# Kernel optimization log

Measured on AMD Instinct MI355X. Metric: run time of the kernel, lower is better.

The kernel has to match this reference:

```python
import jax, jax.numpy as jnp
import numpy as np

DIM = 256
N_EMBED = 8192
DECAY = 0.1
COMMITMENT = 1.0
EPS = 1e-05


def setup_inputs() -> dict:
    key = jax.random.key(0)
    k1, k2, k3, k4 = jax.random.split(key, 4)
    return {
        "input": jax.random.normal(k1, (8, 1024, DIM), dtype=jnp.float32),
        "embed": jax.random.normal(k2, (DIM, N_EMBED), dtype=jnp.float32),
        "cluster_size": jax.random.uniform(k3, (N_EMBED,), dtype=jnp.float32),
        "embed_avg": jax.random.normal(k4, (DIM, N_EMBED), dtype=jnp.float32),
    }


def reference(input, embed, cluster_size, embed_avg):
    dtype = input.dtype
    flatten = input.reshape(-1, DIM)  # [N, dim]
    # squared euclidean distance to each code: [N, n_embed]
    dist = (
        jnp.sum(flatten * flatten, axis=1, keepdims=True)
        - 2.0 * (flatten @ embed)
        + jnp.sum(embed * embed, axis=0, keepdims=True)
    )
    embed_ind_flat = jnp.argmin(dist, axis=1)  # [N]
    embed_ind = embed_ind_flat.reshape(input.shape[:-1])
    quantize = jnp.take(embed.T, embed_ind, axis=0)  # [..., dim]

    # EMA codebook update (training path), via segment sums instead of dense one-hot
    bins = jax.ops.segment_sum(
        jnp.ones_like(embed_ind_flat, dtype=dtype), embed_ind_flat, num_segments=N_EMBED
    )  # one_hot.sum(0)
    embed_sum = jax.ops.segment_sum(flatten, embed_ind_flat, num_segments=N_EMBED).T  # [dim, n_embed]
    cluster_size_new = cluster_size * DECAY + (1.0 - DECAY) * bins
    embed_avg_new = embed_avg * DECAY + (1.0 - DECAY) * embed_sum
    smoothed = (cluster_size_new + EPS) / (jnp.sum(cluster_size_new) + N_EMBED * EPS)
    cs = smoothed * jnp.sum(cluster_size_new)
    embed_normalized = embed_avg_new / cs[None, :]

    commit_loss = jnp.mean((jax.lax.stop_gradient(quantize) - input) ** 2) * COMMITMENT
    quantize_st = input + jax.lax.stop_gradient(quantize - input)
    return (quantize_st, embed_ind, commit_loss, embed_normalized, cluster_size_new, embed_avg_new)
```

## Files before the change

### kernel.cpp

```cpp
#include <hip/hip_runtime.h>

typedef unsigned short u16;
typedef __attribute__((ext_vector_type(8))) short short8;
typedef __attribute__((ext_vector_type(4))) float f32x4;

#define DIM    256
#define NE     8192
#define NROWS  8192
#define DECAY  0.1f
#define EPS_F  1e-5f
#define CRANGES 16
#define CPAIRS  16
#define MQ      384u

#define OUT_Q    0
#define OUT_IND  2097152
#define OUT_LOSS 2105344
#define OUT_NORM 2105345
#define OUT_CSN  4202497
#define OUT_AVG  4210689

#define WS_CAND  65536
#define WS_ENORM 1114112
#define WS_BASEQ 1146880
#define WS_SUM   1179648
#define WS_BINS  9568256
#define WS_LOSS  9601024
#define WS_SCS   9601032
#define WS_XB    9601040
#define WS_ETB   13795344
#define WS_ET32  17989648
#define WS_ZLEN  (WS_XB - WS_SUM)

__device__ __forceinline__ unsigned f32_ord(float f)
{
    unsigned u = __float_as_uint(f);
    return (u & 0x80000000u) ? ~u : (u | 0x80000000u);
}
__device__ __forceinline__ u16 bf16rne(float f)
{
    unsigned u = __float_as_uint(f);
    return (u16)((u + 0x7fffu + ((u >> 16) & 1u)) >> 16);
}
__device__ __forceinline__ void gload16(const void* g, void* l)
{
    __builtin_amdgcn_global_load_lds((const __attribute__((address_space(1))) unsigned int*)g,
                                     (__attribute__((address_space(3))) unsigned int*)l, 16, 0, 0);
}

__global__ __launch_bounds__(256) void vq_prep_k(const float* __restrict__ X,
                                                 const float* __restrict__ E,
                                                 const float* __restrict__ CS,
                                                 u16* __restrict__ Xb,
                                                 float* __restrict__ ET32,
                                                 u16* __restrict__ ETb,
                                                 float* __restrict__ enorm,
                                                 float* __restrict__ baseq,
                                                 double* __restrict__ sumcs)
{
    const int bid = blockIdx.x;
    const int t = threadIdx.x;

    if (bid < 128) {
        __shared__ float T[64][65];
        const int j0 = bid * 64;
        const int jc = t >> 2, seg = t & 3;
        const int j = j0 + jc;
        float esum = 0.f;
        for (int d0 = 0; d0 < DIM; d0 += 64) {
            if (d0) __syncthreads();
            #pragma unroll
            for (int p = 0; p < 4; ++p) {
                const int dr = p * 16 + (t >> 4);
                const float4 v = *(const float4*)(E + (size_t)(d0 + dr) * NE + j0 + (t & 15) * 4);
                T[dr][(t & 15) * 4 + 0] = v.x; T[dr][(t & 15) * 4 + 1] = v.y;
                T[dr][(t & 15) * 4 + 2] = v.z; T[dr][(t & 15) * 4 + 3] = v.w;
            }
            __syncthreads();
            float vals[16];
            #pragma unroll
            for (int i = 0; i < 16; ++i) vals[i] = T[seg * 16 + i][jc];
            float4* o32 = (float4*)(ET32 + (size_t)j * DIM + d0 + seg * 16);
            o32[0] = make_float4(vals[0], vals[1], vals[2], vals[3]);
            o32[1] = make_float4(vals[4], vals[5], vals[6], vals[7]);
            o32[2] = make_float4(vals[8], vals[9], vals[10], vals[11]);
            o32[3] = make_float4(vals[12], vals[13], vals[14], vals[15]);
            short8 b0, b1;
            #pragma unroll
            for (int i = 0; i < 8; ++i) { b0[i] = (short)bf16rne(vals[i]); b1[i] = (short)bf16rne(vals[8 + i]); }
            *(short8*)(ETb + (size_t)j * DIM + d0 + seg * 16) = b0;
            *(short8*)(ETb + (size_t)j * DIM + d0 + seg * 16 + 8) = b1;
            #pragma unroll
            for (int i = 0; i < 16; ++i) esum += vals[i] * vals[i];
        }
        esum += __shfl_xor(esum, 1, 4);
        esum += __shfl_xor(esum, 2, 4);
        if (seg == 0) {
            enorm[j] = esum;
            baseq[j] = (esum + 512.f) * 256.f;
        }
    } else if (bid < 256) {
        const int chunk = bid - 128;
        #pragma unroll
        for (int it = 0; it < 8; ++it) {
            const int gi = chunk * 2048 + it * 256 + t;
            const float4 a = ((const float4*)X)[gi * 2];
            const float4 b = ((const float4*)X)[gi * 2 + 1];
            short8 v;
            v[0] = (short)bf16rne(a.x); v[1] = (short)bf16rne(a.y);
            v[2] = (short)bf16rne(a.z); v[3] = (short)bf16rne(a.w);
            v[4] = (short)bf16rne(b.x); v[5] = (short)bf16rne(b.y);
            v[6] = (short)bf16rne(b.z); v[7] = (short)bf16rne(b.w);
            *(short8*)(Xb + (size_t)gi * 8) = v;
        }
    } else {
        double s = 0.0;
        #pragma unroll
        for (int it = 0; it < 8; ++it) {
            const float4 v = ((const float4*)CS)[it * 256 + t];
            s += (double)v.x + (double)v.y + (double)v.z + (double)v.w;
        }
        #pragma unroll
        for (int off = 32; off > 0; off >>= 1) s += __shfl_down(s, off);
        __shared__ double wred[4];
        if ((t & 63) == 0) wred[t >> 6] = s;
        __syncthreads();
        if (t == 0) sumcs[0] = wred[0] + wred[1] + wred[2] + wred[3];
    }
}

__global__ __launch_bounds__(256, 4) void vq_scan_k(const u16* __restrict__ Xb,
                                                    const u16* __restrict__ ETb,
                                                    const float* __restrict__ baseq,
                                                    unsigned* __restrict__ cand)
{
    __shared__ u16 Bs[2][16][512];

    const int tid = threadIdx.x;
    const int w = tid >> 6, l = tid & 63;
    const int lane16 = l & 15, g = l >> 4;
    const int rowbase = blockIdx.x * 128 + w * 32;
    const int c0 = blockIdx.y * 512;

    short8 af[2][8];
    #pragma unroll
    for (int sub = 0; sub < 2; ++sub)
        #pragma unroll
        for (int k8 = 0; k8 < 8; ++k8) {
            af[sub][k8] = *(const short8*)(Xb + (size_t)(rowbase + sub * 16 + lane16) * DIM + k8 * 32 + g * 8);
            asm volatile("" : "+a"(af[sub][k8]));
        }

    unsigned s0[8], s1[8];
    #pragma unroll
    for (int i = 0; i < 8; ++i) { s0[i] = 0xFFFFFFFFu; s1[i] = 0xFFFFFFFFu; }

    const u16* gsrc = ETb + (size_t)(c0 + lane16) * DIM + (size_t)w * 64 + g * 8;

    gload16(gsrc,                 &Bs[0][2 * w + 0][0]);
    gload16(gsrc + 32,            &Bs[0][2 * w + 1][0]);
    gload16(gsrc + 16 * DIM,      &Bs[0][8 + 2 * w + 0][0]);
    gload16(gsrc + 16 * DIM + 32, &Bs[0][8 + 2 * w + 1][0]);

    int buf = 0;
    #pragma unroll 1
    for (int p = 0; p < CPAIRS; ++p) {
        if (p + 1 < CPAIRS) {
            const u16* nsrc = gsrc + (size_t)(p + 1) * 32 * DIM;
            gload16(nsrc,                 &Bs[buf ^ 1][2 * w + 0][0]);
            gload16(nsrc + 32,            &Bs[buf ^ 1][2 * w + 1][0]);
            gload16(nsrc + 16 * DIM,      &Bs[buf ^ 1][8 + 2 * w + 0][0]);
            gload16(nsrc + 16 * DIM + 32, &Bs[buf ^ 1][8 + 2 * w + 1][0]);
            asm volatile("s_waitcnt vmcnt(4)" ::: "memory");
        } else {
            asm volatile("s_waitcnt vmcnt(0)" ::: "memory");
        }
        __builtin_amdgcn_s_barrier();

        #pragma unroll
        for (int half = 0; half < 2; ++half) {
            const int col = c0 + (p * 2 + half) * 16 + lane16;
            const float bq = baseq[col];
            f32x4 acc[2];
            acc[0] = {0.f, 0.f, 0.f, 0.f};
            acc[1] = {0.f, 0.f, 0.f, 0.f};
            #pragma unroll
            for (int k8 = 0; k8 < 8; ++k8) {
                const short8 bf = *(const short8*)&Bs[buf][half * 8 + k8][l * 8];
                acc[0] = __builtin_amdgcn_mfma_f32_16x16x32_bf16(af[0][k8], bf, acc[0], 0, 0, 0);
                acc[1] = __builtin_amdgcn_mfma_f32_16x16x32_bf16(af[1][k8], bf, acc[1], 0, 0, 0);
            }
            #pragma unroll
            for (int sub = 0; sub < 2; ++sub)
                #pragma unroll
                for (int r = 0; r < 4; ++r) {
                    const int i = sub * 4 + r;
                    const float qf = fmaf(acc[sub][r], -512.f, bq);
                    const unsigned key = (((unsigned)qf) << 13) | (unsigned)col;
                    const unsigned tt = max(s0[i], key);
                    s0[i] = min(s0[i], key);
                    s1[i] = min(s1[i], tt);
                }
        }
        __builtin_amdgcn_s_barrier();
        buf ^= 1;
    }

    #pragma unroll
    for (int m = 1; m < 16; m <<= 1) {
        #pragma unroll
        for (int i = 0; i < 8; ++i) {
            const unsigned o0 = __shfl_xor(s0[i], m);
            const unsigned o1 = __shfl_xor(s1[i], m);
            const unsigned t0 = min(s0[i], o0);
            const unsigned t1 = min(max(s0[i], o0), min(s1[i], o1));
            s0[i] = t0; s1[i] = t1;
        }
    }
    if (lane16 == 0) {
        #pragma unroll
        for (int i = 0; i < 8; ++i) {
            const int row = rowbase + (i >> 2) * 16 + g * 4 + (i & 3);
            cand[((size_t)row * CRANGES + blockIdx.y) * 2 + 0] = s0[i];
            cand[((size_t)row * CRANGES + blockIdx.y) * 2 + 1] = s1[i];
        }
    }
}

__global__ __launch_bounds__(256) void vq_finalize_k(const unsigned* __restrict__ cand,
                                                     const float* __restrict__ X,
                                                     const float* __restrict__ ET32,
                                                     const float* __restrict__ enorm,
                                                     float* __restrict__ out_q,
                                                     float* __restrict__ out_ind,
                                                     float* __restrict__ ws_sum,
                                                     float* __restrict__ bins,
                                                     double* __restrict__ loss)
{
    __shared__ int sj[4];
    const int tid = threadIdx.x;
    const int w = tid >> 6, l = tid & 63;
    const int row = blockIdx.x * 4 + w;

    unsigned key = 0xFFFFFFFFu;
    if (l < 32) key = cand[(size_t)row * 32 + l];
    unsigned qmin = key;
    #pragma unroll
    for (int m = 32; m; m >>= 1) qmin = min(qmin, __shfl_xor(qmin, m));
    const unsigned qthr = (qmin >> 13) + MQ;
    unsigned long long mask = __ballot((l < 32) && ((key >> 13) <= qthr));
    const float4 xv = *(const float4*)(X + (size_t)row * DIM + l * 4);
    unsigned long long best = 0xFFFFFFFFFFFFFFFFull;
    while (mask) {
        const int src = __builtin_ctzll(mask);
        mask &= mask - 1;
        const int col = (int)(__shfl(key, src) & 8191u);
        const float4 ev = *(const float4*)(ET32 + (size_t)col * DIM + l * 4);
        float s = xv.x * ev.x + xv.y * ev.y + xv.z * ev.z + xv.w * ev.w;
        #pragma unroll
        for (int m = 32; m; m >>= 1) s += __shfl_xor(s, m);
        const float d = enorm[col] - 2.f * s;
        const unsigned long long k64 = ((unsigned long long)f32_ord(d) << 32) | (unsigned)col;
        best = (k64 < best) ? k64 : best;
    }
    if (l == 0) {
        const int j = (int)(best & 8191u);
        sj[w] = j;
        out_ind[row] = (float)j;
    }
    __syncthreads();

    float lsum = 0.f;
    #pragma unroll
    for (int q = 0; q < 4; ++q) {
        const int r = blockIdx.x * 4 + q;
        const int j = sj[q];
        const float x  = X[(size_t)r * DIM + tid];
        const float qv = ET32[(size_t)j * DIM + tid];
        out_q[(size_t)r * DIM + tid] = x + (qv - x);
        const float d = qv - x;
        lsum += d * d;
        atomicAdd(&ws_sum[(size_t)j * DIM + tid], x);
        if (tid == 0) atomicAdd(&bins[j], 1.0f);
    }
    #pragma unroll
    for (int off = 32; off > 0; off >>= 1) lsum += __shfl_down(lsum, off);
    __shared__ double wred[4];
    if ((tid & 63) == 0) wred[tid >> 6] = (double)lsum;
    __syncthreads();
    if (tid == 0) atomicAdd(loss, wred[0] + wred[1] + wred[2] + wred[3]);
}

__global__ __launch_bounds__(256) void vq_embed_k(const float* __restrict__ EA,
                                                  const float* __restrict__ cs,
                                                  const float* __restrict__ bins,
                                                  const float* __restrict__ ws_sum,
                                                  const double* __restrict__ sumcs,
                                                  const double* __restrict__ loss,
                                                  float* __restrict__ out_norm,
                                                  float* __restrict__ out_avg,
                                                  float* __restrict__ out_csn,
                                                  float* __restrict__ out_loss)
{
    __shared__ float T[64][69];
    const int tid = threadIdx.x;
    const int j0 = blockIdx.x * 64;
    const int d0 = blockIdx.y * 64;
    #pragma unroll
    for (int p = 0; p < 4; ++p) {
        const int jr = (tid >> 4) + p * 16;
        const int dc = (tid & 15) * 4;
        const float4 v = *(const float4*)(ws_sum + (size_t)(j0 + jr) * DIM + d0 + dc);
        T[jr][dc + 0] = v.x; T[jr][dc + 1] = v.y; T[jr][dc + 2] = v.z; T[jr][dc + 3] = v.w;
    }
    __syncthreads();
    const double S = (double)DECAY * sumcs[0] + (double)(1.0f - DECAY) * (double)NROWS;
    const float fac = (float)(S / (S + (double)NE * 1e-5));
    const int jc = tid & 63;
    const int j  = j0 + jc;
    const float csn  = cs[j] * DECAY + (1.0f - DECAY) * bins[j];
    const float cs_j = (csn + EPS_F) * fac;
    if (blockIdx.y == 0 && tid < 64) out_csn[j0 + tid] = cs[j0 + tid] * DECAY + (1.0f - DECAY) * bins[j0 + tid];
    if (blockIdx.y == 0 && blockIdx.x == 0 && tid == 0) out_loss[0] = (float)(loss[0] * (1.0 / 2097152.0));
    const int drb = (tid >> 6) * 16;
    #pragma unroll
    for (int p = 0; p < 16; ++p) {
        const int dr = drb + p;
        const float sum = T[jc][dr];
        const float ea  = EA[(size_t)(d0 + dr) * NE + j];
        const float ean = DECAY * ea + (1.0f - DECAY) * sum;
        out_avg[(size_t)(d0 + dr) * NE + j]  = ean;
        out_norm[(size_t)(d0 + dr) * NE + j] = ean / cs_j;
    }
}

extern "C" void kernel_launch(void* const* d_in, const int* in_sizes, int n_in,
                              void* d_out, int out_size, void* d_ws, size_t ws_size,
                              hipStream_t stream)
{
    const float* X  = (const float*)d_in[0];
    const float* E  = (const float*)d_in[1];
    const float* CS = (const float*)d_in[2];
    const float* EA = (const float*)d_in[3];
    float* out = (float*)d_out;
    char*  ws  = (char*)d_ws;

    unsigned* cand  = (unsigned*)(ws + WS_CAND);
    float*  enorm  = (float*)(ws + WS_ENORM);
    float*  baseq  = (float*)(ws + WS_BASEQ);
    float*  ws_sum = (float*)(ws + WS_SUM);
    float*  bins   = (float*)(ws + WS_BINS);
    double* loss   = (double*)(ws + WS_LOSS);
    double* sumcs  = (double*)(ws + WS_SCS);
    u16*    Xb     = (u16*)(ws + WS_XB);
    u16*    ETb    = (u16*)(ws + WS_ETB);
    float*  ET32   = (float*)(ws + WS_ET32);

    hipMemsetAsync(ws + WS_SUM, 0, WS_ZLEN, stream);

    vq_prep_k<<<257, 256, 0, stream>>>(X, E, CS, Xb, ET32, ETb, enorm, baseq, sumcs);
    vq_scan_k<<<dim3(NROWS / 128, CRANGES), 256, 0, stream>>>(Xb, ETb, baseq, cand);
    vq_finalize_k<<<NROWS / 4, 256, 0, stream>>>(cand, X, ET32, enorm, out + OUT_Q, out + OUT_IND, ws_sum, bins, loss);
    vq_embed_k<<<dim3(NE / 64, DIM / 64), 256, 0, stream>>>(EA, CS, bins, ws_sum, sumcs, loss,
                                                            out + OUT_NORM, out + OUT_AVG, out + OUT_CSN, out + OUT_LOSS);
}
```

Baseline: 106.6 us.

## Fuse all VQ stages into one cooperative kernel with grid syncs

Replaces the memset plus four separate kernel launches with a single cooperative kernel of 512 blocks that runs prep, scan, finalize and embed-update phases separated by grid.sync(). Zeroing of the accumulation workspace moves into spare blocks of the prep phase. The aim is to remove launch gaps and the separate memset. In exchange, each phase is tied to a fixed 512-block grid with launch bounds of two blocks per unit, which may reduce parallelism or occupancy in some phases, and grid barriers add their own cost. The old multi-kernel path remains as a fallback if the cooperative launch fails.

```diff
diff --git a/kernel.cpp b/kernel.cpp
--- a/kernel.cpp
+++ b/kernel.cpp
@@ -1,4 +1,7 @@
 #include <hip/hip_runtime.h>
+#include <hip/hip_cooperative_groups.h>
+
+namespace cg = cooperative_groups;
 
 typedef unsigned short u16;
 typedef __attribute__((ext_vector_type(8))) short short8;
@@ -31,6 +34,7 @@
 #define WS_ETB   13795344
 #define WS_ET32  17989648
 #define WS_ZLEN  (WS_XB - WS_SUM)
+#define ZERO_F4  ((WS_LOSS - WS_SUM) / 16)
 
 __device__ __forceinline__ unsigned f32_ord(float f)
 {
@@ -47,6 +51,298 @@
     __builtin_amdgcn_global_load_lds((const __attribute__((address_space(1))) unsigned int*)g,
                                      (__attribute__((address_space(3))) unsigned int*)l, 16, 0, 0);
 }
+
+__global__ __launch_bounds__(256, 2) void vq_all_k(const float* __restrict__ X,
+                                                   const float* __restrict__ E,
+                                                   const float* __restrict__ CS,
+                                                   const float* __restrict__ EA,
+                                                   float* __restrict__ out,
+                                                   char* __restrict__ ws)
+{
+    __shared__ union {
+        float T[64][65];
+        u16   Bs[2][16][512];
+        float Temb[64][69];
+        struct { int sj[4]; double wred[4]; } f;
+    } sm;
+
+    unsigned* cand  = (unsigned*)(ws + WS_CAND);
+    float*  enorm  = (float*)(ws + WS_ENORM);
+    float*  baseq  = (float*)(ws + WS_BASEQ);
+    float*  ws_sum = (float*)(ws + WS_SUM);
+    float*  bins   = (float*)(ws + WS_BINS);
+    double* loss   = (double*)(ws + WS_LOSS);
+    double* sumcs  = (double*)(ws + WS_SCS);
+    u16*    Xb     = (u16*)(ws + WS_XB);
+    u16*    ETb    = (u16*)(ws + WS_ETB);
+    float*  ET32   = (float*)(ws + WS_ET32);
+    float*  out_q    = out + OUT_Q;
+    float*  out_ind  = out + OUT_IND;
+    float*  out_loss = out + OUT_LOSS;
+    float*  out_norm = out + OUT_NORM;
+    float*  out_csn  = out + OUT_CSN;
+    float*  out_avg  = out + OUT_AVG;
+
+    const int bid = blockIdx.x;
+    const int t   = threadIdx.x;
+    cg::grid_group grid = cg::this_grid();
+
+    if (bid < 128) {
+        const int j0 = bid * 64;
+        const int jc = t >> 2, seg = t & 3;
+        const int j = j0 + jc;
+        float esum = 0.f;
+        for (int d0 = 0; d0 < DIM; d0 += 64) {
+            if (d0) __syncthreads();
+            #pragma unroll
+            for (int p = 0; p < 4; ++p) {
+                const int dr = p * 16 + (t >> 4);
+                const float4 v = *(const float4*)(E + (size_t)(d0 + dr) * NE + j0 + (t & 15) * 4);
+                sm.T[dr][(t & 15) * 4 + 0] = v.x; sm.T[dr][(t & 15) * 4 + 1] = v.y;
+                sm.T[dr][(t & 15) * 4 + 2] = v.z; sm.T[dr][(t & 15) * 4 + 3] = v.w;
+            }
+            __syncthreads();
+            float vals[16];
+            #pragma unroll
+            for (int i = 0; i < 16; ++i) vals[i] = sm.T[seg * 16 + i][jc];
+            float4* o32 = (float4*)(ET32 + (size_t)j * DIM + d0 + seg * 16);
+            o32[0] = make_float4(vals[0], vals[1], vals[2], vals[3]);
+            o32[1] = make_float4(vals[4], vals[5], vals[6], vals[7]);
+            o32[2] = make_float4(vals[8], vals[9], vals[10], vals[11]);
+            o32[3] = make_float4(vals[12], vals[13], vals[14], vals[15]);
+            short8 b0, b1;
+            #pragma unroll
+            for (int i = 0; i < 8; ++i) { b0[i] = (short)bf16rne(vals[i]); b1[i] = (short)bf16rne(vals[8 + i]); }
+            *(short8*)(ETb + (size_t)j * DIM + d0 + seg * 16) = b0;
+            *(short8*)(ETb + (size_t)j * DIM + d0 + seg * 16 + 8) = b1;
+            #pragma unroll
+            for (int i = 0; i < 16; ++i) esum += vals[i] * vals[i];
+        }
+        esum += __shfl_xor(esum, 1, 4);
+        esum += __shfl_xor(esum, 2, 4);
+        if (seg == 0) {
+            enorm[j] = esum;
+            baseq[j] = (esum + 512.f) * 256.f;
+        }
+    } else if (bid < 384) {
+        const int chunk = bid - 128;
+        #pragma unroll
+        for (int it = 0; it < 4; ++it) {
+            const int gi = chunk * 1024 + it * 256 + t;
+            const float4 a = ((const float4*)X)[gi * 2];
+            const float4 b = ((const float4*)X)[gi * 2 + 1];
+            short8 v;
+            v[0] = (short)bf16rne(a.x); v[1] = (short)bf16rne(a.y);
+            v[2] = (short)bf16rne(a.z); v[3] = (short)bf16rne(a.w);
+            v[4] = (short)bf16rne(b.x); v[5] = (short)bf16rne(b.y);
+            v[6] = (short)bf16rne(b.z); v[7] = (short)bf16rne(b.w);
+            *(short8*)(Xb + (size_t)gi * 8) = v;
+        }
+    } else if (bid == 384) {
+        double s = 0.0;
+        #pragma unroll
+        for (int it = 0; it < 8; ++it) {
+            const float4 v = ((const float4*)CS)[it * 256 + t];
+            s += (double)v.x + (double)v.y + (double)v.z + (double)v.w;
+        }
+        #pragma unroll
+        for (int off = 32; off > 0; off >>= 1) s += __shfl_down(s, off);
+        if ((t & 63) == 0) sm.f.wred[t >> 6] = s;
+        __syncthreads();
+        if (t == 0) {
+            sumcs[0] = sm.f.wred[0] + sm.f.wred[1] + sm.f.wred[2] + sm.f.wred[3];
+            loss[0]  = 0.0;
+        }
+    } else {
+        float4* z = (float4*)(ws + WS_SUM);
+        const float4 zv = make_float4(0.f, 0.f, 0.f, 0.f);
+        for (int i = (bid - 385) * 256 + t; i < ZERO_F4; i += 127 * 256) z[i] = zv;
+    }
+
+    grid.sync();
+
+    {
+        const int w = t >> 6, l = t & 63;
+        const int lane16 = l & 15, g = l >> 4;
+        const int rowbase = (bid >> 4) * 256 + w * 64;
+        const int c0 = (bid & 15) * 512;
+
+        short8 af[4][8];
+        #pragma unroll
+        for (int sub = 0; sub < 4; ++sub)
+            #pragma unroll
+            for (int k8 = 0; k8 < 8; ++k8)
+                af[sub][k8] = *(const short8*)(Xb + (size_t)(rowbase + sub * 16 + lane16) * DIM + k8 * 32 + g * 8);
+
+        unsigned s0[16], s1[16];
+        #pragma unroll
+        for (int i = 0; i < 16; ++i) { s0[i] = 0xFFFFFFFFu; s1[i] = 0xFFFFFFFFu; }
+
+        const u16* gsrc = ETb + (size_t)(c0 + lane16) * DIM + (size_t)w * 64 + g * 8;
+
+        gload16(gsrc,                 &sm.Bs[0][2 * w + 0][0]);
+        gload16(gsrc + 32,            &sm.Bs[0][2 * w + 1][0]);
+        gload16(gsrc + 16 * DIM,      &sm.Bs[0][8 + 2 * w + 0][0]);
+        gload16(gsrc + 16 * DIM + 32, &sm.Bs[0][8 + 2 * w + 1][0]);
+
+        int buf = 0;
+        #pragma unroll 1
+        for (int p = 0; p < CPAIRS; ++p) {
+            if (p + 1 < CPAIRS) {
+                const u16* nsrc = gsrc + (size_t)(p + 1) * 32 * DIM;
+                gload16(nsrc,                 &sm.Bs[buf ^ 1][2 * w + 0][0]);
+                gload16(nsrc + 32,            &sm.Bs[buf ^ 1][2 * w + 1][0]);
+                gload16(nsrc + 16 * DIM,      &sm.Bs[buf ^ 1][8 + 2 * w + 0][0]);
+                gload16(nsrc + 16 * DIM + 32, &sm.Bs[buf ^ 1][8 + 2 * w + 1][0]);
+                asm volatile("s_waitcnt vmcnt(4)" ::: "memory");
+            } else {
+                asm volatile("s_waitcnt vmcnt(0)" ::: "memory");
+            }
+            __builtin_amdgcn_s_barrier();
+
+            #pragma unroll
+            for (int half = 0; half < 2; ++half) {
+                const int col = c0 + (p * 2 + half) * 16 + lane16;
+                const float bq = baseq[col];
+                f32x4 acc[4];
+                #pragma unroll
+                for (int sub = 0; sub < 4; ++sub) acc[sub] = {0.f, 0.f, 0.f, 0.f};
+                #pragma unroll
+                for (int k8 = 0; k8 < 8; ++k8) {
+                    const short8 bf = *(const short8*)&sm.Bs[buf][half * 8 + k8][l * 8];
+                    #pragma unroll
+                    for (int sub = 0; sub < 4; ++sub)
+                        acc[sub] = __builtin_amdgcn_mfma_f32_16x16x32_bf16(af[sub][k8], bf, acc[sub], 0, 0, 0);
+                }
+                #pragma unroll
+                for (int sub = 0; sub < 4; ++sub)
+                    #pragma unroll
+                    for (int r = 0; r < 4; ++r) {
+                        const int i = sub * 4 + r;
+                        const float qf = fmaf(acc[sub][r], -512.f, bq);
+                        const unsigned key = (((unsigned)qf) << 13) | (unsigned)col;
+                        const unsigned tt = max(s0[i], key);
+                        s0[i] = min(s0[i], key);
+                        s1[i] = min(s1[i], tt);
+                    }
+            }
+            __builtin_amdgcn_s_barrier();
+            buf ^= 1;
+        }
+
+        #pragma unroll
+        for (int m = 1; m < 16; m <<= 1) {
+            #pragma unroll
+            for (int i = 0; i < 16; ++i) {
+                const unsigned o0 = __shfl_xor(s0[i], m);
+                const unsigned o1 = __shfl_xor(s1[i], m);
+                const unsigned t0 = min(s0[i], o0);
+                const unsigned t1 = min(max(s0[i], o0), min(s1[i], o1));
+                s0[i] = t0; s1[i] = t1;
+            }
+        }
+        if (lane16 == 0) {
+            #pragma unroll
+            for (int i = 0; i < 16; ++i) {
+                const int row = rowbase + (i >> 2) * 16 + g * 4 + (i & 3);
+                cand[((size_t)row * CRANGES + (bid & 15)) * 2 + 0] = s0[i];
+                cand[((size_t)row * CRANGES + (bid & 15)) * 2 + 1] = s1[i];
+            }
+        }
+    }
+
+    grid.sync();
+
+    {
+        const int w = t >> 6, l = t & 63;
+        float lsum = 0.f;
+        #pragma unroll 1
+        for (int it = 0; it < 4; ++it) {
+            const int rowq = bid * 16 + it * 4;
+            const int row = rowq + w;
+            unsigned key = 0xFFFFFFFFu;
+            if (l < 32) key = cand[(size_t)row * 32 + l];
+            unsigned qmin = key;
+            #pragma unroll
+            for (int m = 32; m; m >>= 1) qmin = min(qmin, __shfl_xor(qmin, m));
+            const unsigned qthr = (qmin >> 13) + MQ;
+            unsigned long long mask = __ballot((l < 32) && ((key >> 13) <= qthr));
+            const float4 xv = *(const float4*)(X + (size_t)row * DIM + l * 4);
+            unsigned long long best = 0xFFFFFFFFFFFFFFFFull;
+            while (mask) {
+                const int src = __builtin_ctzll(mask);
+                mask &= mask - 1;
+                const int col = (int)(__shfl(key, src) & 8191u);
+                const float4 ev = *(const float4*)(ET32 + (size_t)col * DIM + l * 4);
+                float s = xv.x * ev.x + xv.y * ev.y + xv.z * ev.z + xv.w * ev.w;
+                #pragma unroll
+                for (int m = 32; m; m >>= 1) s += __shfl_xor(s, m);
+                const float d = enorm[col] - 2.f * s;
+                const unsigned long long k64 = ((unsigned long long)f32_ord(d) << 32) | (unsigned)col;
+                best = (k64 < best) ? k64 : best;
+            }
+            if (l == 0) {
+                const int j = (int)(best & 8191u);
+                sm.f.sj[w] = j;
+                out_ind[row] = (float)j;
+            }
+            __syncthreads();
+            #pragma unroll
+            for (int q = 0; q < 4; ++q) {
+                const int r = rowq + q;
+                const int j = sm.f.sj[q];
+                const float x  = X[(size_t)r * DIM + t];
+                const float qv = ET32[(size_t)j * DIM + t];
+                out_q[(size_t)r * DIM + t] = x + (qv - x);
+                const float d = qv - x;
+                lsum += d * d;
+                atomicAdd(&ws_sum[(size_t)j * DIM + t], x);
+                if (t == 0) atomicAdd(&bins[j], 1.0f);
+            }
+            __syncthreads();
+        }
+        #pragma unroll
+        for (int off = 32; off > 0; off >>= 1) lsum += __shfl_down(lsum, off);
+        if ((t & 63) == 0) sm.f.wred[t >> 6] = (double)lsum;
+        __syncthreads();
+        if (t == 0) atomicAdd(loss, sm.f.wred[0] + sm.f.wred[1] + sm.f.wred[2] + sm.f.wred[3]);
+    }
+
+    grid.sync();
+
+    {
+        const int xb = bid & 127, yb = bid >> 7;
+        const int j0 = xb * 64, d0 = yb * 64;
+        #pragma unroll
+        for (int p = 0; p < 4; ++p) {
+            const int jr = (t >> 4) + p * 16;
+            const int dc = (t & 15) * 4;
+            const float4 v = *(const float4*)(ws_sum + (size_t)(j0 + jr) * DIM + d0 + dc);
+            sm.Temb[jr][dc + 0] = v.x; sm.Temb[jr][dc + 1] = v.y;
+            sm.Temb[jr][dc + 2] = v.z; sm.Temb[jr][dc + 3] = v.w;
+        }
+        __syncthreads();
+        const double S = (double)DECAY * sumcs[0] + (double)(1.0f - DECAY) * (double)NROWS;
+        const float fac = (float)(S / (S + (double)NE * 1e-5));
+        const int jc = t & 63;
+        const int j  = j0 + jc;
+        const float csn  = CS[j] * DECAY + (1.0f - DECAY) * bins[j];
+        const float cs_j = (csn + EPS_F) * fac;
+        if (yb == 0 && t < 64) out_csn[j0 + t] = CS[j0 + t] * DECAY + (1.0f - DECAY) * bins[j0 + t];
+        if (bid == 0 && t == 0) out_loss[0] = (float)(loss[0] * (1.0 / 2097152.0));
+        const int drb = (t >> 6) * 16;
+        #pragma unroll
+        for (int p = 0; p < 16; ++p) {
+            const int dr = drb + p;
+            const float sum = sm.Temb[jc][dr];
+            const float ea  = EA[(size_t)(d0 + dr) * NE + j];
+            const float ean = DECAY * ea + (1.0f - DECAY) * sum;
+            out_avg[(size_t)(d0 + dr) * NE + j]  = ean;
+            out_norm[(size_t)(d0 + dr) * NE + j] = ean / cs_j;
+        }
+    }
+}
+
 
 __global__ __launch_bounds__(256) void vq_prep_k(const float* __restrict__ X,
                                                  const float* __restrict__ E,
@@ -345,6 +641,11 @@
     float* out = (float*)d_out;
     char*  ws  = (char*)d_ws;
 
+    void* args[] = {(void*)&X, (void*)&E, (void*)&CS, (void*)&EA, (void*)&out, (void*)&ws};
+    hipError_t err = hipLaunchCooperativeKernel(reinterpret_cast<void*>(vq_all_k),
+                                                dim3(512), dim3(256), args, 0, stream);
+    if (err == hipSuccess) return;
+
     unsigned* cand  = (unsigned*)(ws + WS_CAND);
     float*  enorm  = (float*)(ws + WS_ENORM);
     float*  baseq  = (float*)(ws + WS_BASEQ);
```

New measurement: 286.6 us. +168.9%, slower.
